# Kernel tuning notes

Measured on AMD Instinct MI355X. Metric: run time of the kernel, lower is better.

## Reference

```python
import jax, jax.numpy as jnp
import numpy as np

SEQ_LEN = 12
E = 64        # embedding_dim
H = 128       # h_dim
BNK = 1024    # bottleneck_dim
MLP = 1024    # mlp_dim
S, P = 32, 24 # scenes, peds per scene (uniform)
B = S * P


def setup_inputs() -> dict:
    key = jax.random.key(0)
    ks = jax.random.split(key, 24)
    w = lambda k, shape: jax.random.normal(k, shape, jnp.float32) * 0.05
    starts = jnp.arange(S, dtype=jnp.int32) * P
    return {
        'last_pos': jax.random.normal(ks[0], (B, 2), jnp.float32),
        'last_pos_rel': jax.random.normal(ks[1], (B, 2), jnp.float32),
        'h0': jax.random.normal(ks[2], (1, B, H), jnp.float32),
        'c0': jax.random.normal(ks[3], (1, B, H), jnp.float32),
        'seq_start_end': jnp.stack([starts, starts + P], axis=1),
        # decoder spatial embedding Linear(2, E)
        'W_se': w(ks[4], (2, E)), 'b_se': jnp.zeros((E,), jnp.float32),
        # LSTM (num_layers=1), PyTorch gate order i,f,g,o
        'W_ih': w(ks[5], (E, 4 * H)), 'b_ih': jnp.zeros((4 * H,), jnp.float32),
        'W_hh': w(ks[6], (H, 4 * H)), 'b_hh': jnp.zeros((4 * H,), jnp.float32),
        # hidden2pos Linear(H, 2)
        'W_hp': w(ks[7], (H, 2)), 'b_hp': jnp.zeros((2,), jnp.float32),
        # pool_net.spatial_embedding Linear(2, E)
        'W_pse': w(ks[8], (2, E)), 'b_pse': jnp.zeros((E,), jnp.float32),
        # pool_net.mlp_pre_pool [E+H, 512, BNK], ReLU, no batchnorm
        'W_p1': w(ks[9], (E + H, 512)), 'b_p1': jnp.zeros((512,), jnp.float32),
        'W_p2': w(ks[10], (512, BNK)), 'b_p2': jnp.zeros((BNK,), jnp.float32),
        # decoder.mlp [H+BNK, MLP, H], ReLU
        'W_m1': w(ks[11], (H + BNK, MLP)), 'b_m1': jnp.zeros((MLP,), jnp.float32),
        'W_m2': w(ks[12], (MLP, H)), 'b_m2': jnp.zeros((H,), jnp.float32),
    }


def reference(last_pos, last_pos_rel, h0, c0, seq_start_end,
              W_se, b_se, W_ih, b_ih, W_hh, b_hh, W_hp, b_hp,
              W_pse, b_pse, W_p1, b_p1, W_p2, b_p2, W_m1, b_m1, W_m2, b_m2):
    batch = last_pos.shape[0]
    n_scenes = seq_start_end.shape[0]
    peds = batch // n_scenes  # uniform scene sizes
    hdim = h0.shape[-1]

    dec_in0 = last_pos_rel @ W_se + b_se  # (B, E)

    def step(carry, _):
        lpos, dec_in, h, c = carry
        # single-step LSTM, PyTorch gate order i,f,g,o
        gates = dec_in @ W_ih + b_ih + h @ W_hh + b_hh  # (B, 4H)
        i, f, g, o = jnp.split(gates, 4, axis=-1)
        c_new = jax.nn.sigmoid(f) * c + jax.nn.sigmoid(i) * jnp.tanh(g)
        h_new = jax.nn.sigmoid(o) * jnp.tanh(c_new)
        rel_pos = h_new @ W_hp + b_hp            # (B, 2)
        curr_pos = rel_pos + lpos                # (B, 2)
        # --- PoolHiddenNet: pool_h[i] = max_j mlp([emb(pos_j - pos_i), h_j]) per scene ---
        pos = curr_pos.reshape(n_scenes, peds, 2)
        rel = pos[:, None, :, :] - pos[:, :, None, :]         # (S, Pi, Pj, 2), pos_j - pos_i
        emb = rel @ W_pse + b_pse                             # (S, Pi, Pj, E)
        hj = jnp.broadcast_to(h_new.reshape(n_scenes, 1, peds, hdim),
                              (n_scenes, peds, peds, hdim))   # h_j along axis 2
        x = jnp.concatenate([emb, hj], axis=-1)               # (S, Pi, Pj, E+H)
        x = jax.nn.relu(x @ W_p1 + b_p1)
        x = jax.nn.relu(x @ W_p2 + b_p2)                      # (S, Pi, Pj, BNK)
        pool_h = x.max(axis=2).reshape(batch, -1)             # (B, BNK)
        # --- decoder.mlp on [h, pool_h] -> new hidden state ---
        dh = jnp.concatenate([h_new, pool_h], axis=-1)
        dh = jax.nn.relu(dh @ W_m1 + b_m1)
        h_final = jax.nn.relu(dh @ W_m2 + b_m2)               # (B, H)
        dec_in_next = rel_pos @ W_se + b_se
        return (curr_pos, dec_in_next, h_final, c_new), rel_pos

    carry0 = (last_pos, dec_in0, h0[0], c0[0])
    (_, _, h_fin, _), pred_rel = jax.lax.scan(step, carry0, None, length=SEQ_LEN)
    return pred_rel, h_fin[None]  # (T, B, 2), (1, B, H)
```

## Files before the change

### kernel.cpp

```cpp
#include <hip/hip_runtime.h>
#include <math.h>

#define NB 768
#define NS 32
#define NP 24
#define ED 64
#define HD 128
#define G4 512
#define BNKD 1024
#define KM1 1152
#define KG 192
#define TSTEPS 12
#define AR 4
#define BPITCH 516
#define HPITCH 516

typedef __bf16 bf16x8 __attribute__((ext_vector_type(8)));
typedef float f32x4 __attribute__((ext_vector_type(4)));
typedef unsigned short u16x8 __attribute__((ext_vector_type(8)));

__device__ __forceinline__ unsigned short f2bf(float f) {
  unsigned u = __float_as_uint(f);
  u = (u + 0x7FFFu + ((u >> 16) & 1u)) >> 16;
  return (unsigned short)u;
}
__device__ __forceinline__ unsigned pack2bf(float a, float b) {
  return (unsigned)f2bf(a) | ((unsigned)f2bf(b) << 16);
}
__device__ __forceinline__ float bf2f(unsigned short h) {
  return __uint_as_float(((unsigned)h) << 16);
}

__global__ void init_kernel(const float* __restrict__ last_pos,
                            const float* __restrict__ last_pos_rel,
                            const float* __restrict__ c0,
                            const float* __restrict__ W_se,
                            const float* __restrict__ b_se,
                            const float* __restrict__ W_pse,
                            const float* __restrict__ b_pse,
                            const float* __restrict__ W_p1,
                            const float* __restrict__ b_p1,
                            const float* __restrict__ W_p2,
                            const float* __restrict__ W_m1,
                            const float* __restrict__ W_m2,
                            const float* __restrict__ W_ih,
                            const float* __restrict__ W_hh,
                            float* __restrict__ ccar,
                            float* __restrict__ din, float* __restrict__ lpos,
                            float* __restrict__ Wc, float* __restrict__ bc,
                            unsigned short* __restrict__ W2T,
                            unsigned short* __restrict__ W1T,
                            unsigned short* __restrict__ WmT,
                            unsigned short* __restrict__ Wgb,
                            unsigned short* __restrict__ Wp1b) {
  int stride = gridDim.x * blockDim.x;
  int idx0 = blockIdx.x * blockDim.x + threadIdx.x;
  for (int i = idx0; i < NB * HD; i += stride) ccar[i] = c0[i];
  for (int i = idx0; i < NB * 2; i += stride) lpos[i] = last_pos[i];
  for (int i = idx0; i < NB * ED; i += stride) {
    int r = i >> 6, e = i & 63;
    din[i] = b_se[e] + last_pos_rel[2 * r] * W_se[e]
                     + last_pos_rel[2 * r + 1] * W_se[ED + e];
  }
  for (int n = idx0; n < G4; n += stride) {
    float w0 = 0.f, w1 = 0.f, bb = b_p1[n];
    for (int e = 0; e < ED; ++e) {
      float wp = W_p1[e * G4 + n];
      w0 += W_pse[e] * wp;
      w1 += W_pse[ED + e] * wp;
      bb += b_pse[e] * wp;
    }
    Wc[n] = w0; Wc[G4 + n] = w1; bc[n] = bb;
  }
  for (int idx = idx0; idx < 1024 * 64; idx += stride) {
    int n = idx & 1023, k0 = (idx >> 10) << 3;
    unsigned pk0 = pack2bf(W_p2[(k0 + 0) * BNKD + n], W_p2[(k0 + 1) * BNKD + n]);
    unsigned pk1 = pack2bf(W_p2[(k0 + 2) * BNKD + n], W_p2[(k0 + 3) * BNKD + n]);
    unsigned pk2 = pack2bf(W_p2[(k0 + 4) * BNKD + n], W_p2[(k0 + 5) * BNKD + n]);
    unsigned pk3 = pack2bf(W_p2[(k0 + 6) * BNKD + n], W_p2[(k0 + 7) * BNKD + n]);
    *(uint4*)&W2T[n * G4 + k0] = make_uint4(pk0, pk1, pk2, pk3);
  }
  for (int idx = idx0; idx < 1024 * 144; idx += stride) {
    int n = idx & 1023, k0 = (idx >> 10) << 3;
    unsigned pk0 = pack2bf(W_m1[(k0 + 0) * BNKD + n], W_m1[(k0 + 1) * BNKD + n]);
    unsigned pk1 = pack2bf(W_m1[(k0 + 2) * BNKD + n], W_m1[(k0 + 3) * BNKD + n]);
    unsigned pk2 = pack2bf(W_m1[(k0 + 4) * BNKD + n], W_m1[(k0 + 5) * BNKD + n]);
    unsigned pk3 = pack2bf(W_m1[(k0 + 6) * BNKD + n], W_m1[(k0 + 7) * BNKD + n]);
    *(uint4*)&W1T[n * KM1 + k0] = make_uint4(pk0, pk1, pk2, pk3);
  }
  for (int idx = idx0; idx < 128 * 128; idx += stride) {
    int n = idx & 127, k0 = (idx >> 7) << 3;
    unsigned pk0 = pack2bf(W_m2[(k0 + 0) * HD + n], W_m2[(k0 + 1) * HD + n]);
    unsigned pk1 = pack2bf(W_m2[(k0 + 2) * HD + n], W_m2[(k0 + 3) * HD + n]);
    unsigned pk2 = pack2bf(W_m2[(k0 + 4) * HD + n], W_m2[(k0 + 5) * HD + n]);
    unsigned pk3 = pack2bf(W_m2[(k0 + 6) * HD + n], W_m2[(k0 + 7) * HD + n]);
    *(uint4*)&WmT[n * BNKD + k0] = make_uint4(pk0, pk1, pk2, pk3);
  }
  for (int idx = idx0; idx < KG * G4; idx += stride) {
    int k = idx >> 9, n = idx & 511;
    float w = (k < ED) ? W_ih[k * G4 + n] : W_hh[(k - ED) * G4 + n];
    Wgb[idx] = f2bf(w);
  }
  for (int idx = idx0; idx < HD * G4; idx += stride) {
    int k = idx >> 9, n = idx & 511;
    Wp1b[idx] = f2bf(W_p1[(ED + k) * G4 + n]);
  }
}

__global__ __launch_bounds__(256) void step_a(
    const float* __restrict__ hprev, const float* __restrict__ cprev,
    const float* __restrict__ din, const float* __restrict__ lpos_in,
    const unsigned short* __restrict__ Wgb,
    const float* __restrict__ b_ih, const float* __restrict__ b_hh,
    const float* __restrict__ W_hp, const float* __restrict__ b_hp,
    const float* __restrict__ W_se, const float* __restrict__ b_se,
    const unsigned short* __restrict__ Wp1b, const float* __restrict__ bc,
    const float* __restrict__ b_m2,
    unsigned short* __restrict__ mhA, float* __restrict__ cnext,
    float* __restrict__ dnext, float* __restrict__ lpos_out,
    float* __restrict__ Hp1, float* __restrict__ pred_out,
    float* __restrict__ hacc_next, int relu_in) {
  __shared__ float x[AR][192];
  __shared__ float gg[AR][G4];
  __shared__ float hl[AR][HD];
  __shared__ float rp[AR][2];
  int t = threadIdx.x;
  int r0 = blockIdx.x * AR;

  for (int i = t; i < AR * ED; i += 256) { int r = i >> 6, k = i & 63; x[r][k] = din[(r0 + r) * ED + k]; }
  for (int i = t; i < AR * HD; i += 256) {
    int r = i >> 7, k = i & 127;
    float v = hprev[(r0 + r) * HD + k];
    if (relu_in) v = fmaxf(v, 0.f);
    x[r][ED + k] = v;
    hacc_next[(r0 + r) * HD + k] = b_m2[k];
  }
  __syncthreads();

  float acc[AR][2];
#pragma unroll
  for (int r = 0; r < AR; ++r) { acc[r][0] = b_ih[t] + b_hh[t]; acc[r][1] = b_ih[t + 256] + b_hh[t + 256]; }
#pragma unroll 4
  for (int k = 0; k < KG; ++k) {
    float w0 = bf2f(Wgb[k * G4 + t]), w1 = bf2f(Wgb[k * G4 + t + 256]);
#pragma unroll
    for (int r = 0; r < AR; ++r) { float a = x[r][k]; acc[r][0] += a * w0; acc[r][1] += a * w1; }
  }
#pragma unroll
  for (int r = 0; r < AR; ++r) { gg[r][t] = acc[r][0]; gg[r][t + 256] = acc[r][1]; }
  __syncthreads();

  for (int i = t; i < AR * HD; i += 256) {
    int r = i >> 7, k = i & 127;
    float ig = gg[r][k], fg = gg[r][HD + k], gz = gg[r][2 * HD + k], og = gg[r][3 * HD + k];
    float si = 1.f / (1.f + expf(-ig));
    float sf = 1.f / (1.f + expf(-fg));
    float so = 1.f / (1.f + expf(-og));
    float gt = tanhf(gz);
    float c = sf * cprev[(r0 + r) * HD + k] + si * gt;
    float h = so * tanhf(c);
    cnext[(r0 + r) * HD + k] = c;
    mhA[(size_t)(r0 + r) * KM1 + k] = f2bf(h);
    hl[r][k] = h;
  }
  __syncthreads();

  if (t < AR * 2) {
    int r = t >> 1, d = t & 1;
    float s = b_hp[d];
    for (int k = 0; k < HD; ++k) s += hl[r][k] * W_hp[k * 2 + d];
    rp[r][d] = s;
    pred_out[(r0 + r) * 2 + d] = s;
    lpos_out[(r0 + r) * 2 + d] = s + lpos_in[(r0 + r) * 2 + d];
  }
  __syncthreads();

  for (int i = t; i < AR * ED; i += 256) {
    int r = i >> 6, e = i & 63;
    dnext[(r0 + r) * ED + e] = b_se[e] + rp[r][0] * W_se[e] + rp[r][1] * W_se[ED + e];
  }

  float bc0 = bc[t], bc1 = bc[t + 256];
  float acc2[AR][2];
#pragma unroll
  for (int r = 0; r < AR; ++r) { acc2[r][0] = bc0; acc2[r][1] = bc1; }
#pragma unroll 4
  for (int k = 0; k < HD; ++k) {
    float w0 = bf2f(Wp1b[k * G4 + t]), w1 = bf2f(Wp1b[k * G4 + t + 256]);
#pragma unroll
    for (int r = 0; r < AR; ++r) { float a = hl[r][k]; acc2[r][0] += a * w0; acc2[r][1] += a * w1; }
  }
#pragma unroll
  for (int r = 0; r < AR; ++r) {
    Hp1[(r0 + r) * G4 + t] = acc2[r][0];
    Hp1[(r0 + r) * G4 + t + 256] = acc2[r][1];
  }
}

__global__ __launch_bounds__(768, 1) void pool_fused(
    const float* __restrict__ curr_pos, const float* __restrict__ Hp1,
    const float* __restrict__ Wc,
    const unsigned short* __restrict__ W2T, const float* __restrict__ b_p2,
    unsigned short* __restrict__ mhA) {
  __shared__ __align__(16) unsigned short Bl[128 * BPITCH];
  __shared__ __align__(16) unsigned short Hs[24 * HPITCH];
  __shared__ __align__(16) unsigned short wc0b[G4], wc1b[G4];
  __shared__ float psx[NP], psy[NP];
  int t = threadIdx.x;
  int b = blockIdx.x;
  int s = b & 31, nt = b >> 5;
  int n0 = nt * 128;

  for (int idx = t; idx < 128 * 64; idx += 768) {
    int row = idx >> 6, ch = (idx & 63) << 3;
    *(uint4*)&Bl[row * BPITCH + ch] = *(const uint4*)&W2T[(size_t)(n0 + row) * G4 + ch];
  }
  for (int idx = t; idx < 24 * 64; idx += 768) {
    int row = idx >> 6, ch = (idx & 63) << 3;
    const float* src = &Hp1[(size_t)(s * NP + row) * G4 + ch];
    float4 v0 = *(const float4*)src;
    float4 v1 = *(const float4*)(src + 4);
    uint4 pk;
    pk.x = pack2bf(v0.x, v0.y); pk.y = pack2bf(v0.z, v0.w);
    pk.z = pack2bf(v1.x, v1.y); pk.w = pack2bf(v1.z, v1.w);
    *(uint4*)&Hs[row * HPITCH + ch] = pk;
  }
  for (int i = t; i < G4; i += 768) {
    wc0b[i] = f2bf(Wc[i]);
    wc1b[i] = f2bf(Wc[G4 + i]);
  }
  if (t < NP) {
    psx[t] = curr_pos[(s * NP + t) * 2];
    psy[t] = curr_pos[(s * NP + t) * 2 + 1];
  }
  __syncthreads();

  int lane = t & 63, wv = t >> 6;
  int arow = lane & 15, ak = (lane >> 4) * 8, h = lane >> 4;
  int ip = wv;

  float rx[3], ry[3];
  int hoff[3];
#pragma unroll
  for (int f = 0; f < 3; ++f) {
    int m = f * 16 + arow;
    int j = m % 24, g = m / 24;
    rx[f] = psx[j] - psx[ip * 2 + g];
    ry[f] = psy[j] - psy[ip * 2 + g];
    hoff[f] = j * HPITCH + ak;
  }
  int boff[8];
#pragma unroll
  for (int nf = 0; nf < 8; ++nf) boff[nf] = (nf * 16 + arow) * BPITCH + ak;

  f32x4 acc[3][8];
#pragma unroll
  for (int f = 0; f < 3; ++f)
#pragma unroll
    for (int nf = 0; nf < 8; ++nf) acc[f][nf] = (f32x4){0.f, 0.f, 0.f, 0.f};

  for (int kt = 0; kt < 16; ++kt) {
    int k0 = kt * 32;
    u16x8 w0v = *(const u16x8*)&wc0b[k0 + ak];
    u16x8 w1v = *(const u16x8*)&wc1b[k0 + ak];
    bf16x8 af[3];
#pragma unroll
    for (int f = 0; f < 3; ++f) {
      u16x8 hp = *(const u16x8*)&Hs[hoff[f] + k0];
      float rxf = rx[f], ryf = ry[f];
#pragma unroll
      for (int q = 0; q < 8; ++q) {
        float v = bf2f(hp[q]) + rxf * bf2f(w0v[q]) + ryf * bf2f(w1v[q]);
        af[f][q] = (__bf16)fmaxf(v, 0.f);
      }
    }
#pragma unroll
    for (int nf = 0; nf < 8; ++nf) {
      bf16x8 bfr = *(const bf16x8*)&Bl[boff[nf] + k0];
      acc[0][nf] = __builtin_amdgcn_mfma_f32_16x16x32_bf16(af[0], bfr, acc[0][nf], 0, 0, 0);
      acc[1][nf] = __builtin_amdgcn_mfma_f32_16x16x32_bf16(af[1], bfr, acc[1][nf], 0, 0, 0);
      acc[2][nf] = __builtin_amdgcn_mfma_f32_16x16x32_bf16(af[2], bfr, acc[2][nf], 0, 0, 0);
    }
  }

  int iA = s * NP + ip * 2;
#pragma unroll
  for (int nf = 0; nf < 8; ++nf) {
    f32x4 a0 = acc[0][nf], a1 = acc[1][nf], a2 = acc[2][nf];
    float v0 = fmaxf(fmaxf(a0[0], a0[1]), fmaxf(a0[2], a0[3]));
    float v1 = fmaxf(fmaxf(a1[0], a1[1]), fmaxf(a1[2], a1[3]));
    float v2 = fmaxf(fmaxf(a2[0], a2[1]), fmaxf(a2[2], a2[3]));
    v0 = fmaxf(v0, __shfl_xor(v0, 16));
    v1 = fmaxf(v1, __shfl_xor(v1, 16));
    v2 = fmaxf(v2, __shfl_xor(v2, 16));
    float xx = (h < 2) ? fmaxf(v0, v1) : v0;
    xx = fmaxf(xx, __shfl_xor(xx, 32));
    float yy = (h >= 2) ? fmaxf(v2, v1) : v2;
    yy = fmaxf(yy, __shfl_xor(yy, 32));
    int col = n0 + nf * 16 + (lane & 15);
    float bb = b_p2[col];
    xx = fmaxf(xx + bb, 0.f);
    yy = fmaxf(yy + bb, 0.f);
    if (h == 0) mhA[(size_t)iA * KM1 + HD + col] = f2bf(xx);
    if (h == 1) mhA[((size_t)iA + 1) * KM1 + HD + col] = f2bf(yy);
  }
}

__global__ __launch_bounds__(256) void mlp1_fused(
    const unsigned short* __restrict__ mhA,
    const unsigned short* __restrict__ W1T, const float* __restrict__ b_m1,
    const unsigned short* __restrict__ WmT, float* __restrict__ hacc) {
  __shared__ __align__(16) float Pl[32][132];
  int t = threadIdx.x, b = blockIdx.x;
  int mt = b >> 3, nt = b & 7;
  int r0 = mt * 32, n0 = nt * 128;
  int lane = t & 63, wid = t >> 6, wm = wid >> 1, wn = wid & 1;
  int arow = lane & 15, ak = (lane >> 4) * 8;
  int h = lane >> 4;

  f32x4 acc0[4];
#pragma unroll
  for (int nf = 0; nf < 4; ++nf) acc0[nf] = (f32x4){0.f, 0.f, 0.f, 0.f};
  int mrow = r0 + wm * 16 + arow;
  const unsigned short* bp[4];
#pragma unroll
  for (int nf = 0; nf < 4; ++nf)
    bp[nf] = W1T + (size_t)(n0 + wn * 64 + nf * 16 + arow) * KM1 + ak;
  const unsigned short* arow_m = mhA + (size_t)mrow * KM1 + ak;

#pragma unroll 4
  for (int kt = 0; kt < 36; ++kt) {
    bf16x8 a = *(const bf16x8*)(arow_m + kt * 32);
#pragma unroll
    for (int nf = 0; nf < 4; ++nf) {
      bf16x8 bb = *(const bf16x8*)(bp[nf] + kt * 32);
      acc0[nf] = __builtin_amdgcn_mfma_f32_16x16x32_bf16(a, bb, acc0[nf], 0, 0, 0);
    }
  }

#pragma unroll
  for (int nf = 0; nf < 4; ++nf) {
    int colp = wn * 64 + nf * 16 + arow;
    float bb = b_m1[n0 + colp];
#pragma unroll
    for (int rr = 0; rr < 4; ++rr)
      Pl[wm * 16 + h * 4 + rr][colp] = fmaxf(acc0[nf][rr] + bb, 0.f);
  }
  __syncthreads();

  f32x4 acc2[4];
#pragma unroll
  for (int nf = 0; nf < 4; ++nf) acc2[nf] = (f32x4){0.f, 0.f, 0.f, 0.f};
  const unsigned short* b2p[4];
#pragma unroll
  for (int nf = 0; nf < 4; ++nf)
    b2p[nf] = WmT + (size_t)(wn * 64 + nf * 16 + arow) * BNKD + n0 + ak;
  const float* prow = &Pl[wm * 16 + arow][0];

#pragma unroll
  for (int k2 = 0; k2 < 4; ++k2) {
    u16x8 uh, ul;
#pragma unroll
    for (int q = 0; q < 8; ++q) {
      float vv = prow[k2 * 32 + ak + q];
      unsigned short hh = f2bf(vv);
      uh[q] = hh;
      ul[q] = f2bf(vv - bf2f(hh));
    }
    bf16x8 ahi = __builtin_bit_cast(bf16x8, uh);
    bf16x8 alo = __builtin_bit_cast(bf16x8, ul);
#pragma unroll
    for (int nf = 0; nf < 4; ++nf) {
      bf16x8 bb = *(const bf16x8*)(b2p[nf] + k2 * 32);
      acc2[nf] = __builtin_amdgcn_mfma_f32_16x16x32_bf16(ahi, bb, acc2[nf], 0, 0, 0);
      acc2[nf] = __builtin_amdgcn_mfma_f32_16x16x32_bf16(alo, bb, acc2[nf], 0, 0, 0);
    }
  }
#pragma unroll
  for (int nf = 0; nf < 4; ++nf)
#pragma unroll
    for (int rr = 0; rr < 4; ++rr)
      atomicAdd(&hacc[(size_t)(r0 + wm * 16 + h * 4 + rr) * HD + wn * 64 + nf * 16 + arow],
                acc2[nf][rr]);
}

__global__ void final_h(const float* __restrict__ hacc, float* __restrict__ out) {
  int i = blockIdx.x * 256 + threadIdx.x;
  if (i < NB * HD) out[i] = fmaxf(hacc[i], 0.f);
}

extern "C" void kernel_launch(void* const* d_in, const int* in_sizes, int n_in,
                              void* d_out, int out_size, void* d_ws, size_t ws_size,
                              hipStream_t stream) {
  const float* last_pos     = (const float*)d_in[0];
  const float* last_pos_rel = (const float*)d_in[1];
  const float* h0   = (const float*)d_in[2];
  const float* c0   = (const float*)d_in[3];
  const float* W_se = (const float*)d_in[5];
  const float* b_se = (const float*)d_in[6];
  const float* W_ih = (const float*)d_in[7];
  const float* b_ih = (const float*)d_in[8];
  const float* W_hh = (const float*)d_in[9];
  const float* b_hh = (const float*)d_in[10];
  const float* W_hp = (const float*)d_in[11];
  const float* b_hp = (const float*)d_in[12];
  const float* W_pse = (const float*)d_in[13];
  const float* b_pse = (const float*)d_in[14];
  const float* W_p1 = (const float*)d_in[15];
  const float* b_p1 = (const float*)d_in[16];
  const float* W_p2 = (const float*)d_in[17];
  const float* b_p2 = (const float*)d_in[18];
  const float* W_m1 = (const float*)d_in[19];
  const float* b_m1 = (const float*)d_in[20];
  const float* W_m2 = (const float*)d_in[21];
  const float* b_m2 = (const float*)d_in[22];

  float* ws = (float*)d_ws;
  float* hacc[2]  = { ws,           ws + 98304 };
  float* ccar[2]  = { ws + 196608,  ws + 294912 };
  float* din[2]   = { ws + 393216,  ws + 442368 };
  float* lposb[2] = { ws + 491520,  ws + 493056 };
  float* Hp1  = ws + 494592;
  float* Wc   = ws + 887808;
  float* bc   = ws + 888832;
  unsigned short* W2T  = (unsigned short*)(ws + 889344);
  unsigned short* W1T  = (unsigned short*)(ws + 1151488);
  unsigned short* WmT  = (unsigned short*)(ws + 1741312);
  unsigned short* mhA  = (unsigned short*)(ws + 1806848);
  unsigned short* Wgb  = (unsigned short*)(ws + 2249216);
  unsigned short* Wp1b = (unsigned short*)(ws + 2298368);

  float* pred = (float*)d_out;

  init_kernel<<<128, 256, 0, stream>>>(last_pos, last_pos_rel, c0,
                                       W_se, b_se, W_pse, b_pse, W_p1, b_p1,
                                       W_p2, W_m1, W_m2, W_ih, W_hh,
                                       ccar[0], din[0], lposb[0],
                                       Wc, bc, W2T, W1T, WmT, Wgb, Wp1b);

  for (int t = 0; t < TSTEPS; ++t) {
    int a = t & 1, b = (t + 1) & 1;
    step_a<<<NB / AR, 256, 0, stream>>>(
        t == 0 ? h0 : hacc[a], ccar[a], din[a], lposb[a],
        Wgb, b_ih, b_hh, W_hp, b_hp, W_se, b_se, Wp1b, bc, b_m2,
        mhA, ccar[b], din[b], lposb[b], Hp1, pred + t * NB * 2,
        hacc[b], t == 0 ? 0 : 1);
    pool_fused<<<NS * 8, 768, 0, stream>>>(lposb[b], Hp1, Wc, W2T, b_p2, mhA);
    mlp1_fused<<<192, 256, 0, stream>>>(mhA, W1T, b_m1, WmT, hacc[b]);
  }

  final_h<<<384, 256, 0, stream>>>(hacc[0], (float*)d_out + TSTEPS * NB * 2);
}
```

Baseline: 1.167 ms.

## Move hidden2pos and pool first-layer matmul into pool kernel with MFMA

step_a now only computes the LSTM gates and cell update. It runs on twice as many blocks, each covering half the hidden units, and reads weights stored transposed with 8-wide bf16 vector loads. The hidden-to-position projection, the position update and next-step embedding, and the h @ W_p1 product are moved into pool_fused. There h @ W_p1 is computed with bf16 MFMA straight from the bf16 hidden state in mhA, which removes the fp32 Hp1 round-trip through global memory and the serial per-block tail in step_a. In exchange, each of the 8 column-tile blocks per scene recomputes the same Hp1 tile and position projection, adding redundant work and prologue latency before the main pooling MFMA loop.

```diff
diff --git a/kernel.cpp b/kernel.cpp
--- a/kernel.cpp
+++ b/kernel.cpp
@@ -11,7 +11,6 @@
 #define KM1 1152
 #define KG 192
 #define TSTEPS 12
-#define AR 4
 #define BPITCH 516
 #define HPITCH 516
 
@@ -51,8 +50,8 @@
                             unsigned short* __restrict__ W2T,
                             unsigned short* __restrict__ W1T,
                             unsigned short* __restrict__ WmT,
-                            unsigned short* __restrict__ Wgb,
-                            unsigned short* __restrict__ Wp1b) {
+                            unsigned short* __restrict__ Wgbn,
+                            unsigned short* __restrict__ Wp1T2) {
   int stride = gridDim.x * blockDim.x;
   int idx0 = blockIdx.x * blockDim.x + threadIdx.x;
   for (int i = idx0; i < NB * HD; i += stride) ccar[i] = c0[i];
@@ -96,39 +95,47 @@
     unsigned pk3 = pack2bf(W_m2[(k0 + 6) * HD + n], W_m2[(k0 + 7) * HD + n]);
     *(uint4*)&WmT[n * BNKD + k0] = make_uint4(pk0, pk1, pk2, pk3);
   }
-  for (int idx = idx0; idx < KG * G4; idx += stride) {
-    int k = idx >> 9, n = idx & 511;
-    float w = (k < ED) ? W_ih[k * G4 + n] : W_hh[(k - ED) * G4 + n];
-    Wgb[idx] = f2bf(w);
-  }
-  for (int idx = idx0; idx < HD * G4; idx += stride) {
-    int k = idx >> 9, n = idx & 511;
-    Wp1b[idx] = f2bf(W_p1[(ED + k) * G4 + n]);
+  for (int idx = idx0; idx < 512 * 24; idx += stride) {
+    int col = idx / 24, kc = (idx % 24) * 8;
+    unsigned short v[8];
+#pragma unroll
+    for (int q = 0; q < 8; ++q) {
+      int k = kc + q;
+      float w = (k < ED) ? W_ih[k * G4 + col] : W_hh[(k - ED) * G4 + col];
+      v[q] = f2bf(w);
+    }
+    uint4 pk;
+    pk.x = v[0] | (v[1] << 16); pk.y = v[2] | (v[3] << 16);
+    pk.z = v[4] | (v[5] << 16); pk.w = v[6] | (v[7] << 16);
+    *(uint4*)&Wgbn[(size_t)col * KG + kc] = pk;
+  }
+  for (int idx = idx0; idx < 512 * 16; idx += stride) {
+    int n = idx >> 4, kc = (idx & 15) << 3;
+    unsigned short v[8];
+#pragma unroll
+    for (int q = 0; q < 8; ++q) v[q] = f2bf(W_p1[(ED + kc + q) * G4 + n]);
+    uint4 pk;
+    pk.x = v[0] | (v[1] << 16); pk.y = v[2] | (v[3] << 16);
+    pk.z = v[4] | (v[5] << 16); pk.w = v[6] | (v[7] << 16);
+    *(uint4*)&Wp1T2[(size_t)n * HD + kc] = pk;
   }
 }
 
 __global__ __launch_bounds__(256) void step_a(
     const float* __restrict__ hprev, const float* __restrict__ cprev,
-    const float* __restrict__ din, const float* __restrict__ lpos_in,
-    const unsigned short* __restrict__ Wgb,
+    const float* __restrict__ din,
+    const unsigned short* __restrict__ Wgbn,
     const float* __restrict__ b_ih, const float* __restrict__ b_hh,
-    const float* __restrict__ W_hp, const float* __restrict__ b_hp,
-    const float* __restrict__ W_se, const float* __restrict__ b_se,
-    const unsigned short* __restrict__ Wp1b, const float* __restrict__ bc,
     const float* __restrict__ b_m2,
     unsigned short* __restrict__ mhA, float* __restrict__ cnext,
-    float* __restrict__ dnext, float* __restrict__ lpos_out,
-    float* __restrict__ Hp1, float* __restrict__ pred_out,
     float* __restrict__ hacc_next, int relu_in) {
-  __shared__ float x[AR][192];
-  __shared__ float gg[AR][G4];
-  __shared__ float hl[AR][HD];
-  __shared__ float rp[AR][2];
-  int t = threadIdx.x;
-  int r0 = blockIdx.x * AR;
-
-  for (int i = t; i < AR * ED; i += 256) { int r = i >> 6, k = i & 63; x[r][k] = din[(r0 + r) * ED + k]; }
-  for (int i = t; i < AR * HD; i += 256) {
+  __shared__ __align__(16) float x[4][200];
+  __shared__ float gg[4][4][64];
+  int t = threadIdx.x, b = blockIdx.x;
+  int rg = b >> 1, hh = b & 1, r0 = rg * 4;
+
+  { int r = t >> 6, k = t & 63; x[r][k] = din[(r0 + r) * ED + k]; }
+  for (int i = t; i < 4 * HD; i += 256) {
     int r = i >> 7, k = i & 127;
     float v = hprev[(r0 + r) * HD + k];
     if (relu_in) v = fmaxf(v, 0.f);
@@ -137,77 +144,63 @@
   }
   __syncthreads();
 
-  float acc[AR][2];
-#pragma unroll
-  for (int r = 0; r < AR; ++r) { acc[r][0] = b_ih[t] + b_hh[t]; acc[r][1] = b_ih[t + 256] + b_hh[t + 256]; }
-#pragma unroll 4
-  for (int k = 0; k < KG; ++k) {
-    float w0 = bf2f(Wgb[k * G4 + t]), w1 = bf2f(Wgb[k * G4 + t + 256]);
-#pragma unroll
-    for (int r = 0; r < AR; ++r) { float a = x[r][k]; acc[r][0] += a * w0; acc[r][1] += a * w1; }
-  }
-#pragma unroll
-  for (int r = 0; r < AR; ++r) { gg[r][t] = acc[r][0]; gg[r][t + 256] = acc[r][1]; }
+  int gq = t >> 6, c = t & 63;
+  int col = gq * 128 + hh * 64 + c;
+  float bb = b_ih[col] + b_hh[col];
+  float a0 = bb, a1 = bb, a2 = bb, a3 = bb;
+  const unsigned short* wp = Wgbn + (size_t)col * KG;
+#pragma unroll 2
+  for (int kc = 0; kc < KG; kc += 8) {
+    u16x8 wv = *(const u16x8*)(wp + kc);
+    float4 x0a = *(const float4*)&x[0][kc], x0b = *(const float4*)&x[0][kc + 4];
+    float4 x1a = *(const float4*)&x[1][kc], x1b = *(const float4*)&x[1][kc + 4];
+    float4 x2a = *(const float4*)&x[2][kc], x2b = *(const float4*)&x[2][kc + 4];
+    float4 x3a = *(const float4*)&x[3][kc], x3b = *(const float4*)&x[3][kc + 4];
+    float w0 = bf2f(wv[0]), w1 = bf2f(wv[1]), w2 = bf2f(wv[2]), w3 = bf2f(wv[3]);
+    float w4 = bf2f(wv[4]), w5 = bf2f(wv[5]), w6 = bf2f(wv[6]), w7 = bf2f(wv[7]);
+    a0 += x0a.x * w0 + x0a.y * w1 + x0a.z * w2 + x0a.w * w3
+        + x0b.x * w4 + x0b.y * w5 + x0b.z * w6 + x0b.w * w7;
+    a1 += x1a.x * w0 + x1a.y * w1 + x1a.z * w2 + x1a.w * w3
+        + x1b.x * w4 + x1b.y * w5 + x1b.z * w6 + x1b.w * w7;
+    a2 += x2a.x * w0 + x2a.y * w1 + x2a.z * w2 + x2a.w * w3
+        + x2b.x * w4 + x2b.y * w5 + x2b.z * w6 + x2b.w * w7;
+    a3 += x3a.x * w0 + x3a.y * w1 + x3a.z * w2 + x3a.w * w3
+        + x3b.x * w4 + x3b.y * w5 + x3b.z * w6 + x3b.w * w7;
+  }
+  gg[0][gq][c] = a0; gg[1][gq][c] = a1; gg[2][gq][c] = a2; gg[3][gq][c] = a3;
   __syncthreads();
 
-  for (int i = t; i < AR * HD; i += 256) {
-    int r = i >> 7, k = i & 127;
-    float ig = gg[r][k], fg = gg[r][HD + k], gz = gg[r][2 * HD + k], og = gg[r][3 * HD + k];
+  {
+    int r2 = t >> 6, c2 = t & 63, hid = hh * 64 + c2;
+    float ig = gg[r2][0][c2], fg = gg[r2][1][c2];
+    float gz = gg[r2][2][c2], og = gg[r2][3][c2];
     float si = 1.f / (1.f + expf(-ig));
     float sf = 1.f / (1.f + expf(-fg));
     float so = 1.f / (1.f + expf(-og));
     float gt = tanhf(gz);
-    float c = sf * cprev[(r0 + r) * HD + k] + si * gt;
-    float h = so * tanhf(c);
-    cnext[(r0 + r) * HD + k] = c;
-    mhA[(size_t)(r0 + r) * KM1 + k] = f2bf(h);
-    hl[r][k] = h;
-  }
-  __syncthreads();
-
-  if (t < AR * 2) {
-    int r = t >> 1, d = t & 1;
-    float s = b_hp[d];
-    for (int k = 0; k < HD; ++k) s += hl[r][k] * W_hp[k * 2 + d];
-    rp[r][d] = s;
-    pred_out[(r0 + r) * 2 + d] = s;
-    lpos_out[(r0 + r) * 2 + d] = s + lpos_in[(r0 + r) * 2 + d];
-  }
-  __syncthreads();
-
-  for (int i = t; i < AR * ED; i += 256) {
-    int r = i >> 6, e = i & 63;
-    dnext[(r0 + r) * ED + e] = b_se[e] + rp[r][0] * W_se[e] + rp[r][1] * W_se[ED + e];
-  }
-
-  float bc0 = bc[t], bc1 = bc[t + 256];
-  float acc2[AR][2];
-#pragma unroll
-  for (int r = 0; r < AR; ++r) { acc2[r][0] = bc0; acc2[r][1] = bc1; }
-#pragma unroll 4
-  for (int k = 0; k < HD; ++k) {
-    float w0 = bf2f(Wp1b[k * G4 + t]), w1 = bf2f(Wp1b[k * G4 + t + 256]);
-#pragma unroll
-    for (int r = 0; r < AR; ++r) { float a = hl[r][k]; acc2[r][0] += a * w0; acc2[r][1] += a * w1; }
-  }
-#pragma unroll
-  for (int r = 0; r < AR; ++r) {
-    Hp1[(r0 + r) * G4 + t] = acc2[r][0];
-    Hp1[(r0 + r) * G4 + t + 256] = acc2[r][1];
+    float cn = sf * cprev[(r0 + r2) * HD + hid] + si * gt;
+    float hv = so * tanhf(cn);
+    cnext[(r0 + r2) * HD + hid] = cn;
+    mhA[(size_t)(r0 + r2) * KM1 + hid] = f2bf(hv);
   }
 }
 
 __global__ __launch_bounds__(768, 1) void pool_fused(
-    const float* __restrict__ curr_pos, const float* __restrict__ Hp1,
-    const float* __restrict__ Wc,
-    const unsigned short* __restrict__ W2T, const float* __restrict__ b_p2,
+    const float* __restrict__ lpos_in,
+    const float* __restrict__ Wc, const float* __restrict__ bc,
+    const unsigned short* __restrict__ W2T,
+    const unsigned short* __restrict__ Wp1T2,
+    const float* __restrict__ b_p2,
+    const float* __restrict__ W_hp, const float* __restrict__ b_hp,
+    const float* __restrict__ W_se, const float* __restrict__ b_se,
+    float* __restrict__ lpos_out, float* __restrict__ dnext,
+    float* __restrict__ pred_out,
     unsigned short* __restrict__ mhA) {
   __shared__ __align__(16) unsigned short Bl[128 * BPITCH];
   __shared__ __align__(16) unsigned short Hs[24 * HPITCH];
   __shared__ __align__(16) unsigned short wc0b[G4], wc1b[G4];
-  __shared__ float psx[NP], psy[NP];
-  int t = threadIdx.x;
-  int b = blockIdx.x;
+  __shared__ float psx[NP], psy[NP], rpx[NP], rpy[NP];
+  int t = threadIdx.x, b = blockIdx.x;
   int s = b & 31, nt = b >> 5;
   int n0 = nt * 128;
 
@@ -215,30 +208,71 @@
     int row = idx >> 6, ch = (idx & 63) << 3;
     *(uint4*)&Bl[row * BPITCH + ch] = *(const uint4*)&W2T[(size_t)(n0 + row) * G4 + ch];
   }
-  for (int idx = t; idx < 24 * 64; idx += 768) {
-    int row = idx >> 6, ch = (idx & 63) << 3;
-    const float* src = &Hp1[(size_t)(s * NP + row) * G4 + ch];
-    float4 v0 = *(const float4*)src;
-    float4 v1 = *(const float4*)(src + 4);
-    uint4 pk;
-    pk.x = pack2bf(v0.x, v0.y); pk.y = pack2bf(v0.z, v0.w);
-    pk.z = pack2bf(v1.x, v1.y); pk.w = pack2bf(v1.z, v1.w);
-    *(uint4*)&Hs[row * HPITCH + ch] = pk;
-  }
-  for (int i = t; i < G4; i += 768) {
-    wc0b[i] = f2bf(Wc[i]);
-    wc1b[i] = f2bf(Wc[G4 + i]);
-  }
-  if (t < NP) {
-    psx[t] = curr_pos[(s * NP + t) * 2];
-    psy[t] = curr_pos[(s * NP + t) * 2 + 1];
-  }
-  __syncthreads();
+  for (int i = t; i < G4; i += 768) { wc0b[i] = f2bf(Wc[i]); wc1b[i] = f2bf(Wc[G4 + i]); }
+
+  {
+    int row = t >> 5, d = (t >> 4) & 1, kc = t & 15;
+    const unsigned short* hr = mhA + (size_t)(s * NP + row) * KM1 + kc * 8;
+    float p = 0.f;
+#pragma unroll
+    for (int q = 0; q < 8; ++q) p += bf2f(hr[q]) * W_hp[(kc * 8 + q) * 2 + d];
+    p += __shfl_xor(p, 1); p += __shfl_xor(p, 2);
+    p += __shfl_xor(p, 4); p += __shfl_xor(p, 8);
+    if (kc == 0) {
+      float rel = p + b_hp[d];
+      float cur = rel + lpos_in[(s * NP + row) * 2 + d];
+      if (d == 0) { rpx[row] = rel; psx[row] = cur; }
+      else        { rpy[row] = rel; psy[row] = cur; }
+    }
+  }
 
   int lane = t & 63, wv = t >> 6;
   int arow = lane & 15, ak = (lane >> 4) * 8, h = lane >> 4;
+
+  for (int pass = 0; pass < 2; ++pass) {
+    if (pass == 1 && wv >= 4) break;
+    int task = (pass == 0) ? wv : 12 + wv;
+    int mf = task >> 3, cg = task & 7;
+    int m = mf * 16 + arow; if (m > 23) m = 23;
+    const unsigned short* ap = mhA + (size_t)(s * NP + m) * KM1 + ak;
+    f32x4 hacc4[4];
+#pragma unroll
+    for (int nf = 0; nf < 4; ++nf) hacc4[nf] = (f32x4){0.f, 0.f, 0.f, 0.f};
+#pragma unroll
+    for (int kt = 0; kt < 4; ++kt) {
+      bf16x8 a = *(const bf16x8*)(ap + kt * 32);
+#pragma unroll
+      for (int nf = 0; nf < 4; ++nf) {
+        bf16x8 bb = *(const bf16x8*)(Wp1T2 + (size_t)(cg * 64 + nf * 16 + arow) * HD + kt * 32 + ak);
+        hacc4[nf] = __builtin_amdgcn_mfma_f32_16x16x32_bf16(a, bb, hacc4[nf], 0, 0, 0);
+      }
+    }
+#pragma unroll
+    for (int nf = 0; nf < 4; ++nf) {
+      int col = cg * 64 + nf * 16 + arow;
+      float bcv = bc[col];
+#pragma unroll
+      for (int rr = 0; rr < 4; ++rr) {
+        int row = mf * 16 + h * 4 + rr;
+        if (row < 24) Hs[row * HPITCH + col] = f2bf(hacc4[nf][rr] + bcv);
+      }
+    }
+  }
+  __syncthreads();
+
+  if (nt == 0) {
+    if (t < 48) {
+      int row = t >> 1, d = t & 1;
+      pred_out[(s * NP + row) * 2 + d] = d ? rpy[row] : rpx[row];
+      lpos_out[(s * NP + row) * 2 + d] = d ? psy[row] : psx[row];
+    }
+    for (int idx = t; idx < NP * ED; idx += 768) {
+      int row = idx >> 6, e = idx & 63;
+      dnext[(s * NP + row) * ED + e] = b_se[e] + rpx[row] * W_se[e] + rpy[row] * W_se[ED + e];
+    }
+  }
+
   int ip = wv;
-
   float rx[3], ry[3];
   int hoff[3];
 #pragma unroll
@@ -298,9 +332,9 @@
     float yy = (h >= 2) ? fmaxf(v2, v1) : v2;
     yy = fmaxf(yy, __shfl_xor(yy, 32));
     int col = n0 + nf * 16 + (lane & 15);
-    float bb = b_p2[col];
-    xx = fmaxf(xx + bb, 0.f);
-    yy = fmaxf(yy + bb, 0.f);
+    float bb2 = b_p2[col];
+    xx = fmaxf(xx + bb2, 0.f);
+    yy = fmaxf(yy + bb2, 0.f);
     if (h == 0) mhA[(size_t)iA * KM1 + HD + col] = f2bf(xx);
     if (h == 1) mhA[((size_t)iA + 1) * KM1 + HD + col] = f2bf(yy);
   }
@@ -420,15 +454,14 @@
   float* ccar[2]  = { ws + 196608,  ws + 294912 };
   float* din[2]   = { ws + 393216,  ws + 442368 };
   float* lposb[2] = { ws + 491520,  ws + 493056 };
-  float* Hp1  = ws + 494592;
-  float* Wc   = ws + 887808;
-  float* bc   = ws + 888832;
-  unsigned short* W2T  = (unsigned short*)(ws + 889344);
-  unsigned short* W1T  = (unsigned short*)(ws + 1151488);
-  unsigned short* WmT  = (unsigned short*)(ws + 1741312);
-  unsigned short* mhA  = (unsigned short*)(ws + 1806848);
-  unsigned short* Wgb  = (unsigned short*)(ws + 2249216);
-  unsigned short* Wp1b = (unsigned short*)(ws + 2298368);
+  float* Wc   = ws + 494592;
+  float* bc   = ws + 495616;
+  unsigned short* W2T   = (unsigned short*)(ws + 496128);
+  unsigned short* W1T   = (unsigned short*)(ws + 758272);
+  unsigned short* WmT   = (unsigned short*)(ws + 1348096);
+  unsigned short* mhA   = (unsigned short*)(ws + 1413632);
+  unsigned short* Wgbn  = (unsigned short*)(ws + 1856000);
+  unsigned short* Wp1T2 = (unsigned short*)(ws + 1905152);
 
   float* pred = (float*)d_out;
 
@@ -436,16 +469,17 @@
                                        W_se, b_se, W_pse, b_pse, W_p1, b_p1,
                                        W_p2, W_m1, W_m2, W_ih, W_hh,
                                        ccar[0], din[0], lposb[0],
-                                       Wc, bc, W2T, W1T, WmT, Wgb, Wp1b);
+                                       Wc, bc, W2T, W1T, WmT, Wgbn, Wp1T2);
 
   for (int t = 0; t < TSTEPS; ++t) {
     int a = t & 1, b = (t + 1) & 1;
-    step_a<<<NB / AR, 256, 0, stream>>>(
-        t == 0 ? h0 : hacc[a], ccar[a], din[a], lposb[a],
-        Wgb, b_ih, b_hh, W_hp, b_hp, W_se, b_se, Wp1b, bc, b_m2,
-        mhA, ccar[b], din[b], lposb[b], Hp1, pred + t * NB * 2,
-        hacc[b], t == 0 ? 0 : 1);
-    pool_fused<<<NS * 8, 768, 0, stream>>>(lposb[b], Hp1, Wc, W2T, b_p2, mhA);
+    step_a<<<384, 256, 0, stream>>>(
+        t == 0 ? h0 : hacc[a], ccar[a], din[a],
+        Wgbn, b_ih, b_hh, b_m2,
+        mhA, ccar[b], hacc[b], t == 0 ? 0 : 1);
+    pool_fused<<<NS * 8, 768, 0, stream>>>(
+        lposb[a], Wc, bc, W2T, Wp1T2, b_p2, W_hp, b_hp, W_se, b_se,
+        lposb[b], din[b], pred + t * NB * 2, mhA);
     mlp1_fused<<<192, 256, 0, stream>>>(mhA, W1T, b_m1, WmT, hacc[b]);
   }
 
```

Result: faster. 1.131 ms (-3.1%).
